# Performance work log

Measured on AMD Instinct MI355X. Metric: run time of the kernel, lower is better.

## Reference

```python
import jax, jax.numpy as jnp
import numpy as np

KH, KW = 3, 3
KN = KH * KW  # kernel_n = 9


def _grid_offset(H, W):
    # Faithful to TF build(): stack(meshgrid(ij)).reshape(-1, 2) -- note this
    # interleaves i- and j- grids in an unusual layout; we replicate it exactly.
    init = jnp.stack(jnp.meshgrid(jnp.arange(KH), jnp.arange(KW), indexing='ij'))
    init = init.reshape(-1, 2).astype(jnp.float32)  # (KN, 2)
    ph, pw = (KH - 1) // 2, (KW - 1) // 2
    g = jnp.stack(
        jnp.meshgrid(jnp.arange(-ph, H - ph), jnp.arange(-pw, W - pw), indexing='ij'),
        axis=-1,
    ).astype(jnp.float32)  # (H, W, 2)
    return g[:, :, None, :] + init[None, None]  # (H, W, KN, 2)


def _bilinear_sample(x, coords):
    # x: (B, H, W, C); coords: (B, H, W, KN, 2) with (row, col) float coords.
    B = x.shape[0]
    y, xc = coords[..., 0], coords[..., 1]
    y0 = jnp.floor(y).astype(jnp.int32)
    y1 = jnp.ceil(y).astype(jnp.int32)   # ceil (not floor+1), faithful to TF code
    x0 = jnp.floor(xc).astype(jnp.int32)
    x1 = jnp.ceil(xc).astype(jnp.int32)
    bidx = jnp.arange(B)[:, None, None, None]

    def g(yy, xx):
        return x[bidx, yy, xx]  # (B, H, W, KN, C)

    v_lt = g(y0, x0)
    v_rb = g(y1, x1)
    v_lb = g(y0, x1)  # (lt_row, rb_col) per TF coords_lb
    v_rt = g(y1, x0)  # (rb_row, lt_col) per TF coords_rt
    fy = (y - y0.astype(y.dtype))[..., None]
    fx = (xc - x0.astype(xc.dtype))[..., None]
    v_t = v_lt + (v_rt - v_lt) * fy
    v_b = v_lb + (v_rb - v_lb) * fy
    return v_t + (v_b - v_t) * fx  # (B, H, W, KN, C)


def setup_inputs() -> dict:
    key = jax.random.key(0)
    k1, k2, k3 = jax.random.split(key, 3)
    B, H, W, C, F = 8, 64, 64, 128, 128
    x = jax.random.normal(k1, (B, H, W, C), dtype=jnp.float32)
    offset = jax.random.normal(k2, (B, H, W, 2 * KN), dtype=jnp.float32)
    Wk = jax.random.truncated_normal(k3, -2.0, 2.0, (KN, C, F), dtype=jnp.float32) * 0.02
    b = jnp.zeros((F,), dtype=jnp.float32)
    return {"x": x, "offset": offset, "W": Wk, "b": b}


def reference(x, offset, W, b):
    B, H, Wd, C = x.shape
    coords = _grid_offset(H, Wd)[None] + offset.reshape(B, H, Wd, KN, 2)
    coords = jnp.stack(
        [
            jnp.clip(coords[..., 0], 0.0, float(H - 1)),
            jnp.clip(coords[..., 1], 0.0, float(Wd - 1)),
        ],
        axis=-1,
    )
    deform = _bilinear_sample(x, coords)  # (B, H, W, KN, C)
    # conv3d with (1,1,KN,C,F) filter, VALID == contraction over (KN, C)
    out = jnp.einsum('bhwnc,ncf->bhwf', deform, W) + b
    return out
```

## Files before the change

### kernel.cpp

```cpp
#include <hip/hip_runtime.h>
#include <stdint.h>

#define KN 9
#define HH 64
#define WW 64
#define CC 128
#define FF 128
#define TM 64
#define NT 512
#define LDK 136

typedef __bf16 bf16x8 __attribute__((ext_vector_type(8)));
typedef float f32x4 __attribute__((ext_vector_type(4)));
typedef unsigned short us8 __attribute__((ext_vector_type(8)));

__constant__ float c_init_i[KN] = {0.f,0.f,1.f,2.f,2.f,1.f,0.f,2.f,1.f};
__constant__ float c_init_j[KN] = {0.f,1.f,1.f,2.f,0.f,2.f,1.f,0.f,2.f};

static __device__ inline unsigned short f2bf(float f) {
    union { float f; unsigned u; } v; v.f = f;
    unsigned r = v.u + 0x7fffu + ((v.u >> 16) & 1u);
    return (unsigned short)(r >> 16);
}

__global__ void wt_kernel(const float* __restrict__ Wk, unsigned short* __restrict__ Wt) {
    __shared__ unsigned short t[32][33];
    const int tid = threadIdx.x;
    const int n  = blockIdx.x >> 4;
    const int tf = blockIdx.x & 3;
    const int tc = (blockIdx.x >> 2) & 3;
    const int g  = tid >> 5;
    const int l  = tid & 31;
#pragma unroll
    for (int r = 0; r < 4; ++r) {
        int cl = g * 4 + r;
        t[cl][l] = f2bf(Wk[(n << 14) + ((tc * 32 + cl) << 7) + (tf * 32 + l)]);
    }
    __syncthreads();
#pragma unroll
    for (int r = 0; r < 4; ++r) {
        int fl = g * 4 + r;
        Wt[(n << 14) + (tc << 12) + ((tf * 32 + fl) << 5) + l] = t[l][fl];
    }
}

__launch_bounds__(NT, 4)
__global__ void deform_kernel(const float* __restrict__ xin,
                              const float* __restrict__ off,
                              const unsigned short* __restrict__ Wt,
                              const float* __restrict__ bias,
                              float* __restrict__ out) {
    __shared__ unsigned short As[TM][LDK];
    __shared__ int   cB[TM][KN][4];
    __shared__ float cF[TM][KN][2];

    const int tid = threadIdx.x;
    const int bb   = blockIdx.x & 7;
    const int hh   = blockIdx.x >> 3;
    const int pix0 = (bb << 12) + (hh << 6);

    for (int t = tid; t < TM * KN; t += NT) {
        int p = t & (TM - 1);
        int n = t >> 6;
        const float* op = off + (size_t)(pix0 + p) * (2 * KN) + 2 * n;
        float y = (float)(hh - 1) + c_init_i[n] + op[0];
        float x = (float)(p - 1) + c_init_j[n] + op[1];
        y = fminf(fmaxf(y, 0.f), 63.f);
        x = fminf(fmaxf(x, 0.f), 63.f);
        float y0f = floorf(y), x0f = floorf(x);
        int y0 = (int)y0f, x0 = (int)x0f;
        int y1 = (int)ceilf(y), x1 = (int)ceilf(x);
        cB[p][n][0] = ((y0 << 6) + x0) << 7;
        cB[p][n][1] = ((y1 << 6) + x0) << 7;
        cB[p][n][2] = ((y0 << 6) + x1) << 7;
        cB[p][n][3] = ((y1 << 6) + x1) << 7;
        cF[p][n][0] = y - y0f;
        cF[p][n][1] = x - x0f;
    }

    const int wave = tid >> 6;
    const int lane = tid & 63;
    const int quad = lane >> 4;
    const int col  = lane & 15;
    const int mtile = (wave & 1) * 32;
    const int ntile = (wave >> 1) * 32;

    f32x4 acc[2][2];
#pragma unroll
    for (int a = 0; a < 2; ++a)
#pragma unroll
        for (int b = 0; b < 2; ++b) acc[a][b] = (f32x4){0.f, 0.f, 0.f, 0.f};

    const float* bbase = xin + ((size_t)bb << 19);
    const unsigned short* wb0 = Wt + ((ntile + col) << 5) + (quad << 3);

    const int ip0 = tid >> 4;
    const int ip1 = ip0 + 32;
    const int icg = (tid & 15) * 8;

    auto issue = [&](int n, int p, float4* pf) {
        int4 cb = *(const int4*)&cB[p][n][0];
        const float* c0 = bbase + cb.x + icg;
        const float* c1 = bbase + cb.y + icg;
        const float* c2 = bbase + cb.z + icg;
        const float* c3 = bbase + cb.w + icg;
        pf[0] = *(const float4*)c0; pf[1] = *(const float4*)(c0 + 4);
        pf[2] = *(const float4*)c1; pf[3] = *(const float4*)(c1 + 4);
        pf[4] = *(const float4*)c2; pf[5] = *(const float4*)(c2 + 4);
        pf[6] = *(const float4*)c3; pf[7] = *(const float4*)(c3 + 4);
    };
    auto consume = [&](int n, int p, const float4* pf) {
        float fy = cF[p][n][0], fx = cF[p][n][1];
        us8 pk;
#pragma unroll
        for (int j = 0; j < 8; ++j) {
            float v0 = pf[0 + (j >> 2)][j & 3];
            float v1 = pf[2 + (j >> 2)][j & 3];
            float v2 = pf[4 + (j >> 2)][j & 3];
            float v3 = pf[6 + (j >> 2)][j & 3];
            float vt = v0 + (v1 - v0) * fy;
            float vb = v2 + (v3 - v2) * fy;
            float r  = vt + (vb - vt) * fx;
            pk[j] = __builtin_bit_cast(unsigned short, (__bf16)r);
        }
        *(us8*)&As[p][icg] = pk;
    };

    __syncthreads();

    float4 pf0[8], pf1[8];
    us8 bfr[8];
    issue(0, ip0, pf0);

    for (int n = 0; n < KN; ++n) {
        const unsigned short* wn = wb0 + (n << 14);
#pragma unroll
        for (int ks = 0; ks < 4; ++ks) {
            bfr[ks * 2]     = *(const us8*)(wn + (ks << 12));
            bfr[ks * 2 + 1] = *(const us8*)(wn + (ks << 12) + (16 << 5));
        }
        issue(n, ip1, pf1);
        consume(n, ip0, pf0);
        consume(n, ip1, pf1);
        __syncthreads();

        if (n + 1 < KN) issue(n + 1, ip0, pf0);

#pragma unroll
        for (int ks = 0; ks < 4; ++ks) {
            bf16x8 a0 = __builtin_bit_cast(bf16x8, *(const us8*)(&As[mtile + col][ks * 32 + quad * 8]));
            bf16x8 a1 = __builtin_bit_cast(bf16x8, *(const us8*)(&As[mtile + 16 + col][ks * 32 + quad * 8]));
            bf16x8 b0 = __builtin_bit_cast(bf16x8, bfr[ks * 2]);
            bf16x8 b1 = __builtin_bit_cast(bf16x8, bfr[ks * 2 + 1]);
            acc[0][0] = __builtin_amdgcn_mfma_f32_16x16x32_bf16(a0, b0, acc[0][0], 0, 0, 0);
            acc[0][1] = __builtin_amdgcn_mfma_f32_16x16x32_bf16(a0, b1, acc[0][1], 0, 0, 0);
            acc[1][0] = __builtin_amdgcn_mfma_f32_16x16x32_bf16(a1, b0, acc[1][0], 0, 0, 0);
            acc[1][1] = __builtin_amdgcn_mfma_f32_16x16x32_bf16(a1, b1, acc[1][1], 0, 0, 0);
        }
        __syncthreads();
    }

#pragma unroll
    for (int b = 0; b < 2; ++b) {
        int f = ntile + b * 16 + col;
        float bv = bias[f];
#pragma unroll
        for (int a = 0; a < 2; ++a) {
#pragma unroll
            for (int r = 0; r < 4; ++r) {
                int pr = pix0 + mtile + a * 16 + quad * 4 + r;
                out[(size_t)pr * FF + f] = acc[a][b][r] + bv;
            }
        }
    }
}

extern "C" void kernel_launch(void* const* d_in, const int* in_sizes, int n_in,
                              void* d_out, int out_size, void* d_ws, size_t ws_size,
                              hipStream_t stream) {
    const float* x    = (const float*)d_in[0];
    const float* off  = (const float*)d_in[1];
    const float* Wk   = (const float*)d_in[2];
    const float* bias = (const float*)d_in[3];
    float* out = (float*)d_out;
    unsigned short* Wt = (unsigned short*)d_ws;

    wt_kernel<<<KN * 16, 256, 0, stream>>>(Wk, Wt);
    deform_kernel<<<(8 * HH * WW) / TM, NT, 0, stream>>>(x, off, Wt, bias, out);
}
```

Baseline: 110.2 us.

## Double-buffer A tile in LDS and interleave gather loads with bilinear compute

Splits the shared A tile into two buffers so each iteration needs a single barrier instead of two. Each thread now handles 4 channels across 4 pixel rows, and the code alternates issue and consume steps with sched barriers to keep gathers in flight while interpolating. The offset reads become float2 loads, and the accumulators are held in scalar variables. This adds LDS usage and relies on manual scheduling hints, which could lower occupancy or hurt the compiler's own scheduling.

```diff
diff --git a/kernel.cpp b/kernel.cpp
--- a/kernel.cpp
+++ b/kernel.cpp
@@ -13,6 +13,7 @@
 typedef __bf16 bf16x8 __attribute__((ext_vector_type(8)));
 typedef float f32x4 __attribute__((ext_vector_type(4)));
 typedef unsigned short us8 __attribute__((ext_vector_type(8)));
+typedef unsigned short us4 __attribute__((ext_vector_type(4)));
 
 __constant__ float c_init_i[KN] = {0.f,0.f,1.f,2.f,2.f,1.f,0.f,2.f,1.f};
 __constant__ float c_init_j[KN] = {0.f,1.f,1.f,2.f,0.f,2.f,1.f,0.f,2.f};
@@ -44,13 +45,45 @@
     }
 }
 
+#define ISSUE(n_, p_, S) do {                                          \
+    int4 cb_ = *(const int4*)&cB[p_][n_][0];                           \
+    lt##S = *(const float4*)(bbase + cb_.x + icg);                     \
+    rt##S = *(const float4*)(bbase + cb_.y + icg);                     \
+    lb##S = *(const float4*)(bbase + cb_.z + icg);                     \
+    rb##S = *(const float4*)(bbase + cb_.w + icg);                     \
+    __builtin_amdgcn_sched_barrier(0);                                 \
+  } while (0)
+
+#define CONSUME(n_, p_, S) do {                                        \
+    float fy_ = cF[p_][n_][0], fx_ = cF[p_][n_][1];                    \
+    us4 pk_;                                                           \
+    _Pragma("unroll")                                                  \
+    for (int j = 0; j < 4; ++j) {                                      \
+      float v0_ = lt##S[j], v1_ = rt##S[j], v2_ = lb##S[j], v3_ = rb##S[j]; \
+      float vt_ = v0_ + (v1_ - v0_) * fy_;                             \
+      float vb_ = v2_ + (v3_ - v2_) * fy_;                             \
+      float r_  = vt_ + (vb_ - vt_) * fx_;                             \
+      pk_[j] = __builtin_bit_cast(unsigned short, (__bf16)r_);         \
+    }                                                                  \
+    *(us4*)&As[d][p_][icg] = pk_;                                      \
+  } while (0)
+
+#define MSTEP(ks_, B0, B1) do {                                        \
+    bf16x8 a0_ = __builtin_bit_cast(bf16x8, *(const us8*)(&As[d][mtile + col][(ks_) * 32 + quad * 8]));      \
+    bf16x8 a1_ = __builtin_bit_cast(bf16x8, *(const us8*)(&As[d][mtile + 16 + col][(ks_) * 32 + quad * 8])); \
+    acc00 = __builtin_amdgcn_mfma_f32_16x16x32_bf16(a0_, __builtin_bit_cast(bf16x8, B0), acc00, 0, 0, 0);    \
+    acc01 = __builtin_amdgcn_mfma_f32_16x16x32_bf16(a0_, __builtin_bit_cast(bf16x8, B1), acc01, 0, 0, 0);    \
+    acc10 = __builtin_amdgcn_mfma_f32_16x16x32_bf16(a1_, __builtin_bit_cast(bf16x8, B0), acc10, 0, 0, 0);    \
+    acc11 = __builtin_amdgcn_mfma_f32_16x16x32_bf16(a1_, __builtin_bit_cast(bf16x8, B1), acc11, 0, 0, 0);    \
+  } while (0)
+
 __launch_bounds__(NT, 4)
 __global__ void deform_kernel(const float* __restrict__ xin,
                               const float* __restrict__ off,
                               const unsigned short* __restrict__ Wt,
                               const float* __restrict__ bias,
                               float* __restrict__ out) {
-    __shared__ unsigned short As[TM][LDK];
+    __shared__ unsigned short As[2][TM][LDK];
     __shared__ int   cB[TM][KN][4];
     __shared__ float cF[TM][KN][2];
 
@@ -62,9 +95,9 @@
     for (int t = tid; t < TM * KN; t += NT) {
         int p = t & (TM - 1);
         int n = t >> 6;
-        const float* op = off + (size_t)(pix0 + p) * (2 * KN) + 2 * n;
-        float y = (float)(hh - 1) + c_init_i[n] + op[0];
-        float x = (float)(p - 1) + c_init_j[n] + op[1];
+        float2 o = *(const float2*)(off + (size_t)(pix0 + p) * (2 * KN) + 2 * n);
+        float y = (float)(hh - 1) + c_init_i[n] + o.x;
+        float x = (float)(p - 1) + c_init_j[n] + o.y;
         y = fminf(fmaxf(y, 0.f), 63.f);
         x = fminf(fmaxf(x, 0.f), 63.f);
         float y0f = floorf(y), x0f = floorf(x);
@@ -85,92 +118,67 @@
     const int mtile = (wave & 1) * 32;
     const int ntile = (wave >> 1) * 32;
 
-    f32x4 acc[2][2];
-#pragma unroll
-    for (int a = 0; a < 2; ++a)
-#pragma unroll
-        for (int b = 0; b < 2; ++b) acc[a][b] = (f32x4){0.f, 0.f, 0.f, 0.f};
+    f32x4 acc00 = {0.f,0.f,0.f,0.f}, acc01 = {0.f,0.f,0.f,0.f};
+    f32x4 acc10 = {0.f,0.f,0.f,0.f}, acc11 = {0.f,0.f,0.f,0.f};
 
     const float* bbase = xin + ((size_t)bb << 19);
     const unsigned short* wb0 = Wt + ((ntile + col) << 5) + (quad << 3);
 
-    const int ip0 = tid >> 4;
-    const int ip1 = ip0 + 32;
-    const int icg = (tid & 15) * 8;
+    const int ip  = tid >> 5;
+    const int icg = (tid & 31) * 4;
 
-    auto issue = [&](int n, int p, float4* pf) {
-        int4 cb = *(const int4*)&cB[p][n][0];
-        const float* c0 = bbase + cb.x + icg;
-        const float* c1 = bbase + cb.y + icg;
-        const float* c2 = bbase + cb.z + icg;
-        const float* c3 = bbase + cb.w + icg;
-        pf[0] = *(const float4*)c0; pf[1] = *(const float4*)(c0 + 4);
-        pf[2] = *(const float4*)c1; pf[3] = *(const float4*)(c1 + 4);
-        pf[4] = *(const float4*)c2; pf[5] = *(const float4*)(c2 + 4);
-        pf[6] = *(const float4*)c3; pf[7] = *(const float4*)(c3 + 4);
-    };
-    auto consume = [&](int n, int p, const float4* pf) {
-        float fy = cF[p][n][0], fx = cF[p][n][1];
-        us8 pk;
-#pragma unroll
-        for (int j = 0; j < 8; ++j) {
-            float v0 = pf[0 + (j >> 2)][j & 3];
-            float v1 = pf[2 + (j >> 2)][j & 3];
-            float v2 = pf[4 + (j >> 2)][j & 3];
-            float v3 = pf[6 + (j >> 2)][j & 3];
-            float vt = v0 + (v1 - v0) * fy;
-            float vb = v2 + (v3 - v2) * fy;
-            float r  = vt + (vb - vt) * fx;
-            pk[j] = __builtin_bit_cast(unsigned short, (__bf16)r);
-        }
-        *(us8*)&As[p][icg] = pk;
-    };
+    float4 ltA, rtA, lbA, rbA;
+    float4 ltB, rtB, lbB, rbB;
+    us8 bfr0, bfr1, bfr2, bfr3, bfr4, bfr5, bfr6, bfr7;
 
     __syncthreads();
 
-    float4 pf0[8], pf1[8];
-    us8 bfr[8];
-    issue(0, ip0, pf0);
+    int d = 0;
+    ISSUE(0, ip, A);
 
-    for (int n = 0; n < KN; ++n) {
+    for (int n = 0; n < KN; ++n, d ^= 1) {
         const unsigned short* wn = wb0 + (n << 14);
-#pragma unroll
-        for (int ks = 0; ks < 4; ++ks) {
-            bfr[ks * 2]     = *(const us8*)(wn + (ks << 12));
-            bfr[ks * 2 + 1] = *(const us8*)(wn + (ks << 12) + (16 << 5));
-        }
-        issue(n, ip1, pf1);
-        consume(n, ip0, pf0);
-        consume(n, ip1, pf1);
-        __syncthreads();
+        bfr0 = *(const us8*)(wn);
+        bfr1 = *(const us8*)(wn + 512);
+        bfr2 = *(const us8*)(wn + 4096);
+        bfr3 = *(const us8*)(wn + 4096 + 512);
+        bfr4 = *(const us8*)(wn + 8192);
+        bfr5 = *(const us8*)(wn + 8192 + 512);
+        bfr6 = *(const us8*)(wn + 12288);
+        bfr7 = *(const us8*)(wn + 12288 + 512);
+        __builtin_amdgcn_sched_barrier(0);
 
-        if (n + 1 < KN) issue(n + 1, ip0, pf0);
+        ISSUE(n, ip + 16, B);
+        CONSUME(n, ip, A);
+        ISSUE(n, ip + 32, A);
+        CONSUME(n, ip + 16, B);
+        ISSUE(n, ip + 48, B);
+        CONSUME(n, ip + 32, A);
+        CONSUME(n, ip + 48, B);
 
-#pragma unroll
-        for (int ks = 0; ks < 4; ++ks) {
-            bf16x8 a0 = __builtin_bit_cast(bf16x8, *(const us8*)(&As[mtile + col][ks * 32 + quad * 8]));
-            bf16x8 a1 = __builtin_bit_cast(bf16x8, *(const us8*)(&As[mtile + 16 + col][ks * 32 + quad * 8]));
-            bf16x8 b0 = __builtin_bit_cast(bf16x8, bfr[ks * 2]);
-            bf16x8 b1 = __builtin_bit_cast(bf16x8, bfr[ks * 2 + 1]);
-            acc[0][0] = __builtin_amdgcn_mfma_f32_16x16x32_bf16(a0, b0, acc[0][0], 0, 0, 0);
-            acc[0][1] = __builtin_amdgcn_mfma_f32_16x16x32_bf16(a0, b1, acc[0][1], 0, 0, 0);
-            acc[1][0] = __builtin_amdgcn_mfma_f32_16x16x32_bf16(a1, b0, acc[1][0], 0, 0, 0);
-            acc[1][1] = __builtin_amdgcn_mfma_f32_16x16x32_bf16(a1, b1, acc[1][1], 0, 0, 0);
-        }
-        __syncthreads();
+        asm volatile("s_waitcnt lgkmcnt(0)" ::: "memory");
+        __builtin_amdgcn_s_barrier();
+
+        if (n + 1 < KN) ISSUE(n + 1, ip, A);
+
+        MSTEP(0, bfr0, bfr1);
+        MSTEP(1, bfr2, bfr3);
+        MSTEP(2, bfr4, bfr5);
+        MSTEP(3, bfr6, bfr7);
     }
 
 #pragma unroll
     for (int b = 0; b < 2; ++b) {
         int f = ntile + b * 16 + col;
         float bv = bias[f];
+        const f32x4 ac0 = b ? acc01 : acc00;
+        const f32x4 ac1 = b ? acc11 : acc10;
 #pragma unroll
-        for (int a = 0; a < 2; ++a) {
-#pragma unroll
-            for (int r = 0; r < 4; ++r) {
-                int pr = pix0 + mtile + a * 16 + quad * 4 + r;
-                out[(size_t)pr * FF + f] = acc[a][b][r] + bv;
-            }
+        for (int r = 0; r < 4; ++r) {
+            int pr0 = pix0 + mtile + quad * 4 + r;
+            out[(size_t)pr0 * FF + f] = ac0[r] + bv;
+            int pr1 = pr0 + 16;
+            out[(size_t)pr1 * FF + f] = ac1[r] + bv;
         }
     }
 }
```

After: 112.3 us. No clear change (+2.0%).
